# Kernel optimization log

Measured on AMD Instinct MI355X. Metric: run time of the kernel, lower is better.

The kernel has to match this reference:

```python
import jax, jax.numpy as jnp
import numpy as np

LEAK = 0.1
EPS = 1e-5


def setup_inputs() -> dict:
    key = jax.random.key(0)
    k1, k2, k3 = jax.random.split(key, 3)
    b, num1, num2, d_in, d_out, n_edges = 8, 4096, 4096, 256, 256, 262144
    N = num1 + num2
    x = jax.random.normal(k1, (b, N, d_in), dtype=jnp.float32)
    W = jax.random.normal(k2, (d_in, d_out), dtype=jnp.float32)
    edges = jax.random.randint(k3, (n_edges, 2), 0, N, dtype=jnp.int64)
    gamma = jnp.ones((d_out,), dtype=jnp.float32)   # LayerNorm weight
    beta = jnp.zeros((d_out,), dtype=jnp.float32)   # LayerNorm bias
    return {"x": x, "W": W, "gamma": gamma, "beta": beta,
            "edges": edges, "num1": num1, "num2": num2}


def reference(x, W, gamma, beta, edges, num1, num2):
    N = num1 + num2
    d_in, d_out = W.shape
    # edges2matrix: scatter 1.0 at (src, dst); duplicates just overwrite (set)
    adj = jnp.zeros((N, N), dtype=x.dtype).at[edges[:, 0], edges[:, 1]].set(1.0)
    # x <- A @ (x @ W), adjacency broadcast over batch
    h = jnp.einsum('nm,bmd->bnd', adj, x @ W)
    if d_out <= d_in:  # LeakyReLU(0.1) branch (static config)
        h = jnp.where(h >= 0, h, LEAK * h)
    # LayerNorm over last dim
    mean = jnp.mean(h, axis=-1, keepdims=True)
    var = jnp.var(h, axis=-1, keepdims=True)
    return gamma * (h - mean) * jax.lax.rsqrt(var + EPS) + beta
```

## Files before the change

### kernel.cpp

```cpp
#include <hip/hip_runtime.h>

#define N_NODES 8192
#define D 256
#define B 8
#define MAXDEG 128

typedef __attribute__((ext_vector_type(8))) short bf16x8;
typedef __attribute__((ext_vector_type(4))) float f32x4;
typedef __attribute__((ext_vector_type(4))) unsigned int u32x4;

static __device__ __forceinline__ float bf2f(unsigned short u) {
    union { float f; unsigned int i; } v; v.i = ((unsigned int)u) << 16; return v.f;
}
static __device__ __forceinline__ float bflo(unsigned int u) {
    union { float f; unsigned int i; } v; v.i = u << 16; return v.f;
}
static __device__ __forceinline__ float bfhi(unsigned int u) {
    union { float f; unsigned int i; } v; v.i = u & 0xFFFF0000u; return v.f;
}
static __device__ __forceinline__ unsigned short f2bf(float f) {
    union { float f; unsigned int i; } v; v.f = f;
    unsigned int r = v.i + 0x7FFFu + ((v.i >> 16) & 1u);
    return (unsigned short)(r >> 16);
}

__global__ __launch_bounds__(256) void build_csr(const int* __restrict__ edges,
        unsigned int* __restrict__ bitmask, int* __restrict__ deg,
        int* __restrict__ adj, int n_edges) {
    int i = blockIdx.x * 256 + threadIdx.x;
    if (i >= n_edges) return;
    int src = edges[2 * i];
    int dst = edges[2 * i + 1];
    unsigned int bitpos = (unsigned int)src * N_NODES + (unsigned int)dst;
    unsigned int bit = 1u << (bitpos & 31u);
    unsigned int old = atomicOr(&bitmask[bitpos >> 5], bit);
    if (!(old & bit)) {
        int slot = atomicAdd(&deg[src], 1);
        if (slot < MAXDEG) adj[src * MAXDEG + slot] = dst;
    }
}

__global__ __launch_bounds__(256) void convert_wt(const float* __restrict__ W,
        unsigned short* __restrict__ Wt) {
    int idx = blockIdx.x * 256 + threadIdx.x;
    int n = idx >> 8, k = idx & 255;
    Wt[n * 256 + k] = f2bf(W[k * 256 + n]);
}

#define GBM 128
__global__ __launch_bounds__(512) void gemm_mfma(const float* __restrict__ x,
        const unsigned short* __restrict__ Wt, unsigned short* __restrict__ xWb) {
    __shared__ alignas(16) char AsB[128 * 128];
    __shared__ alignas(16) char WsB[256 * 128];
    const int t = threadIdx.x;
    const int l = t & 63;
    const int w = t >> 6;
    const int wr = w >> 2;
    const int wc = w & 3;
    const size_t m0 = (size_t)blockIdx.x * GBM;

    f32x4 acc[4][4];
#pragma unroll
    for (int i = 0; i < 4; ++i)
#pragma unroll
        for (int j = 0; j < 4; ++j) acc[i][j] = (f32x4){0.f, 0.f, 0.f, 0.f};

    for (int ks = 0; ks < 4; ++ks) {
        const int k0 = ks * 64;
#pragma unroll
        for (int p = 0; p < 4; ++p) {
            const int row = p * 32 + (t >> 4);
            const int c4  = t & 15;
            float4 v = *(const float4*)&x[(m0 + row) * 256 + k0 + c4 * 4];
            uint2 pk;
            pk.x = (unsigned)f2bf(v.x) | ((unsigned)f2bf(v.y) << 16);
            pk.y = (unsigned)f2bf(v.z) | ((unsigned)f2bf(v.w) << 16);
            const int g = c4 >> 1;
            *(uint2*)&AsB[row * 128 + ((g ^ (row & 7)) * 16) + (c4 & 1) * 8] = pk;
        }
#pragma unroll
        for (int p = 0; p < 4; ++p) {
            const int rp = p * 64 + w * 8 + (l >> 3);
            const int sg = (l & 7) ^ (rp & 7);
            const unsigned short* gp = Wt + rp * 256 + k0 + sg * 8;
            char* lp = &WsB[p * 8192 + w * 1024];
            __builtin_amdgcn_global_load_lds(
                (__attribute__((address_space(1))) unsigned int*)gp,
                (__attribute__((address_space(3))) unsigned int*)lp, 16, 0, 0);
        }
        __syncthreads();
#pragma unroll
        for (int kc = 0; kc < 2; ++kc) {
            bf16x8 xa[4], wb[4];
#pragma unroll
            for (int fm = 0; fm < 4; ++fm) {
                const int row = wr * 64 + fm * 16 + (l & 15);
                const int g = kc * 4 + (l >> 4);
                xa[fm] = *(const bf16x8*)&AsB[row * 128 + ((g ^ (row & 7)) * 16)];
            }
#pragma unroll
            for (int fn = 0; fn < 4; ++fn) {
                const int n = wc * 64 + fn * 16 + (l & 15);
                const int g = kc * 4 + (l >> 4);
                wb[fn] = *(const bf16x8*)&WsB[n * 128 + ((g ^ (n & 7)) * 16)];
            }
#pragma unroll
            for (int fm = 0; fm < 4; ++fm)
#pragma unroll
                for (int fn = 0; fn < 4; ++fn)
                    acc[fm][fn] = __builtin_amdgcn_mfma_f32_16x16x32_bf16(
                        wb[fn], xa[fm], acc[fm][fn], 0, 0, 0);
        }
        __syncthreads();
    }
#pragma unroll
    for (int fm = 0; fm < 4; ++fm) {
        const size_t m = m0 + wr * 64 + fm * 16 + (l & 15);
        unsigned short* rowp = xWb + m * 256 + wc * 64 + (l >> 4) * 4;
#pragma unroll
        for (int fn = 0; fn < 4; ++fn) {
            f32x4 v = acc[fm][fn];
            uint2 pk;
            pk.x = (unsigned)f2bf(v.x) | ((unsigned)f2bf(v.y) << 16);
            pk.y = (unsigned)f2bf(v.z) | ((unsigned)f2bf(v.w) << 16);
            *(uint2*)(rowp + fn * 16) = pk;
        }
    }
}

__global__ __launch_bounds__(512) void gather_ln(const unsigned short* __restrict__ xWb,
        const int* __restrict__ deg, const int* __restrict__ adj,
        const float* __restrict__ gamma, const float* __restrict__ beta,
        float* __restrict__ out) {
    const int bid = blockIdx.x;
    const int batch = bid & 7;
    const int w = threadIdx.x >> 6;
    const int l = threadIdx.x & 63;
    const int half = l >> 5;
    const int sl = l & 31;
    const int n = (bid >> 3) * 8 + w;

    __shared__ int off[8][MAXDEG];
    int dg = deg[n];
    dg = dg > MAXDEG ? MAXDEG : dg;
    for (int i = l; i < dg; i += 64)
        off[w][i] = adj[n * MAXDEG + i] << 9;
    __syncthreads();

    const char* base = (const char*)xWb + (size_t)batch * (N_NODES * D * 2) + sl * 16;
    f32x4 a0 = {0.f, 0.f, 0.f, 0.f}, a1 = {0.f, 0.f, 0.f, 0.f};
    int i = 0;
#pragma unroll 2
    for (; i + 2 <= dg; i += 2) {
        u32x4 v = *(const u32x4*)(base + off[w][i + half]);
        f32x4 c0, c1;
        c0.x = bflo(v.x); c0.y = bfhi(v.x); c0.z = bflo(v.y); c0.w = bfhi(v.y);
        c1.x = bflo(v.z); c1.y = bfhi(v.z); c1.z = bflo(v.w); c1.w = bfhi(v.w);
        a0 += c0;
        a1 += c1;
    }
    if (i < dg && half == 0) {
        u32x4 v = *(const u32x4*)(base + off[w][i]);
        f32x4 c0, c1;
        c0.x = bflo(v.x); c0.y = bfhi(v.x); c0.z = bflo(v.y); c0.w = bfhi(v.y);
        c1.x = bflo(v.z); c1.y = bfhi(v.z); c1.z = bflo(v.w); c1.w = bfhi(v.w);
        a0 += c0;
        a1 += c1;
    }
    a0.x += __shfl_xor(a0.x, 32); a0.y += __shfl_xor(a0.y, 32);
    a0.z += __shfl_xor(a0.z, 32); a0.w += __shfl_xor(a0.w, 32);
    a1.x += __shfl_xor(a1.x, 32); a1.y += __shfl_xor(a1.y, 32);
    a1.z += __shfl_xor(a1.z, 32); a1.w += __shfl_xor(a1.w, 32);
    a0.x = a0.x >= 0.f ? a0.x : 0.1f * a0.x;
    a0.y = a0.y >= 0.f ? a0.y : 0.1f * a0.y;
    a0.z = a0.z >= 0.f ? a0.z : 0.1f * a0.z;
    a0.w = a0.w >= 0.f ? a0.w : 0.1f * a0.w;
    a1.x = a1.x >= 0.f ? a1.x : 0.1f * a1.x;
    a1.y = a1.y >= 0.f ? a1.y : 0.1f * a1.y;
    a1.z = a1.z >= 0.f ? a1.z : 0.1f * a1.z;
    a1.w = a1.w >= 0.f ? a1.w : 0.1f * a1.w;
    float s = (a0.x + a0.y + a0.z + a0.w) + (a1.x + a1.y + a1.z + a1.w);
    float q = (a0.x * a0.x + a0.y * a0.y + a0.z * a0.z + a0.w * a0.w)
            + (a1.x * a1.x + a1.y * a1.y + a1.z * a1.z + a1.w * a1.w);
#pragma unroll
    for (int o = 1; o < 32; o <<= 1) {
        s += __shfl_xor(s, o);
        q += __shfl_xor(q, o);
    }
    const float mean = s * (1.f / D);
    const float var  = q * (1.f / D) - mean * mean;
    const float rstd = rsqrtf(var + 1e-5f);
    f32x4 sel = half ? a1 : a0;
    const int col = sl * 8 + half * 4;
    float4 g  = *(const float4*)(gamma + col);
    float4 bt = *(const float4*)(beta + col);
    f32x4 o4;
    o4.x = g.x * (sel.x - mean) * rstd + bt.x;
    o4.y = g.y * (sel.y - mean) * rstd + bt.y;
    o4.z = g.z * (sel.z - mean) * rstd + bt.z;
    o4.w = g.w * (sel.w - mean) * rstd + bt.w;
    __builtin_nontemporal_store(o4,
        (f32x4*)(out + ((size_t)batch * N_NODES + n) * D + col));
}

extern "C" void kernel_launch(void* const* d_in, const int* in_sizes, int n_in,
                              void* d_out, int out_size, void* d_ws, size_t ws_size,
                              hipStream_t stream) {
    const float* x     = (const float*)d_in[0];
    const float* W     = (const float*)d_in[1];
    const float* gamma = (const float*)d_in[2];
    const float* beta  = (const float*)d_in[3];
    const int*   edges = (const int*)d_in[4];
    const int n_edges  = in_sizes[4] / 2;

    char* ws = (char*)d_ws;
    int*            degp    = (int*)ws;
    unsigned int*   bitmask = (unsigned int*)(ws + 32768);
    int*            adj     = (int*)(ws + 32768 + 8388608);
    unsigned short* xWb     = (unsigned short*)(ws + 32768 + 8388608 + 4194304);
    unsigned short* Wt      = (unsigned short*)(ws + 32768);

    (void)hipMemsetAsync(d_ws, 0, 32768 + 8388608, stream);

    build_csr<<<(n_edges + 255) / 256, 256, 0, stream>>>(edges, bitmask, degp, adj, n_edges);
    convert_wt<<<256, 256, 0, stream>>>(W, Wt);
    gemm_mfma<<<(B * N_NODES) / GBM, 512, 0, stream>>>(x, Wt, xWb);
    gather_ln<<<N_NODES, 512, 0, stream>>>(xWb, degp, adj, gamma, beta, (float*)d_out);
}
```

Measured before the change: 221.4 us.

## Pre-convert x to bf16 and load GEMM A tiles via direct global-to-LDS

Adds a separate convert_x kernel that writes x as bf16 into the output buffer, used as scratch. The GEMM can then stream A tiles with global_load_lds instead of loading fp32 and converting in registers. The gather kernel now stores neighbor offsets split by parity, so each half-wave walks its own list in a single unrolled loop with no tail branch. The cost is an extra kernel launch and an extra full pass over x: an fp32 read and a bf16 write, then a bf16 re-read.

```diff
diff --git a/kernel.cpp b/kernel.cpp
--- a/kernel.cpp
+++ b/kernel.cpp
@@ -9,19 +9,16 @@
 typedef __attribute__((ext_vector_type(4))) float f32x4;
 typedef __attribute__((ext_vector_type(4))) unsigned int u32x4;
 
-static __device__ __forceinline__ float bf2f(unsigned short u) {
-    union { float f; unsigned int i; } v; v.i = ((unsigned int)u) << 16; return v.f;
-}
 static __device__ __forceinline__ float bflo(unsigned int u) {
     union { float f; unsigned int i; } v; v.i = u << 16; return v.f;
 }
 static __device__ __forceinline__ float bfhi(unsigned int u) {
     union { float f; unsigned int i; } v; v.i = u & 0xFFFF0000u; return v.f;
 }
-static __device__ __forceinline__ unsigned short f2bf(float f) {
+static __device__ __forceinline__ unsigned int f2bf(float f) {
     union { float f; unsigned int i; } v; v.f = f;
     unsigned int r = v.i + 0x7FFFu + ((v.i >> 16) & 1u);
-    return (unsigned short)(r >> 16);
+    return r >> 16;
 }
 
 __global__ __launch_bounds__(256) void build_csr(const int* __restrict__ edges,
@@ -44,11 +41,24 @@
         unsigned short* __restrict__ Wt) {
     int idx = blockIdx.x * 256 + threadIdx.x;
     int n = idx >> 8, k = idx & 255;
-    Wt[n * 256 + k] = f2bf(W[k * 256 + n]);
+    Wt[n * 256 + k] = (unsigned short)f2bf(W[k * 256 + n]);
+}
+
+__global__ __launch_bounds__(256) void convert_x(const float* __restrict__ x,
+        unsigned short* __restrict__ xb) {
+    size_t i = ((size_t)blockIdx.x * 256 + threadIdx.x) * 8;
+    float4 v0 = *(const float4*)(x + i);
+    float4 v1 = *(const float4*)(x + i + 4);
+    u32x4 o;
+    o.x = f2bf(v0.x) | (f2bf(v0.y) << 16);
+    o.y = f2bf(v0.z) | (f2bf(v0.w) << 16);
+    o.z = f2bf(v1.x) | (f2bf(v1.y) << 16);
+    o.w = f2bf(v1.z) | (f2bf(v1.w) << 16);
+    *(u32x4*)(xb + i) = o;
 }
 
 #define GBM 128
-__global__ __launch_bounds__(512) void gemm_mfma(const float* __restrict__ x,
+__global__ __launch_bounds__(512) void gemm_mfma(const unsigned short* __restrict__ xb,
         const unsigned short* __restrict__ Wt, unsigned short* __restrict__ xWb) {
     __shared__ alignas(16) char AsB[128 * 128];
     __shared__ alignas(16) char WsB[256 * 128];
@@ -68,15 +78,14 @@
     for (int ks = 0; ks < 4; ++ks) {
         const int k0 = ks * 64;
 #pragma unroll
-        for (int p = 0; p < 4; ++p) {
-            const int row = p * 32 + (t >> 4);
-            const int c4  = t & 15;
-            float4 v = *(const float4*)&x[(m0 + row) * 256 + k0 + c4 * 4];
-            uint2 pk;
-            pk.x = (unsigned)f2bf(v.x) | ((unsigned)f2bf(v.y) << 16);
-            pk.y = (unsigned)f2bf(v.z) | ((unsigned)f2bf(v.w) << 16);
-            const int g = c4 >> 1;
-            *(uint2*)&AsB[row * 128 + ((g ^ (row & 7)) * 16) + (c4 & 1) * 8] = pk;
+        for (int p = 0; p < 2; ++p) {
+            const int row = p * 64 + w * 8 + (l >> 3);
+            const int sg = (l & 7) ^ (row & 7);
+            const unsigned short* gp = xb + (m0 + row) * 256 + k0 + sg * 8;
+            char* lp = &AsB[p * 8192 + w * 1024];
+            __builtin_amdgcn_global_load_lds(
+                (__attribute__((address_space(1))) unsigned int*)gp,
+                (__attribute__((address_space(3))) unsigned int*)lp, 16, 0, 0);
         }
 #pragma unroll
         for (int p = 0; p < 4; ++p) {
@@ -121,8 +130,8 @@
         for (int fn = 0; fn < 4; ++fn) {
             f32x4 v = acc[fm][fn];
             uint2 pk;
-            pk.x = (unsigned)f2bf(v.x) | ((unsigned)f2bf(v.y) << 16);
-            pk.y = (unsigned)f2bf(v.z) | ((unsigned)f2bf(v.w) << 16);
+            pk.x = f2bf(v.x) | (f2bf(v.y) << 16);
+            pk.y = f2bf(v.z) | (f2bf(v.w) << 16);
             *(uint2*)(rowp + fn * 16) = pk;
         }
     }
@@ -140,27 +149,20 @@
     const int sl = l & 31;
     const int n = (bid >> 3) * 8 + w;
 
-    __shared__ int off[8][MAXDEG];
+    __shared__ int off[8][2][64];
     int dg = deg[n];
     dg = dg > MAXDEG ? MAXDEG : dg;
     for (int i = l; i < dg; i += 64)
-        off[w][i] = adj[n * MAXDEG + i] << 9;
+        off[w][i & 1][i >> 1] = adj[n * MAXDEG + i] << 9;
     __syncthreads();
 
-    const char* base = (const char*)xWb + (size_t)batch * (N_NODES * D * 2) + sl * 16;
+    const char* slab = (const char*)xWb + (size_t)batch * (N_NODES * D * 2);
+    const int sl16 = sl * 16;
+    const int jn = (dg - half + 1) >> 1;
     f32x4 a0 = {0.f, 0.f, 0.f, 0.f}, a1 = {0.f, 0.f, 0.f, 0.f};
-    int i = 0;
-#pragma unroll 2
-    for (; i + 2 <= dg; i += 2) {
-        u32x4 v = *(const u32x4*)(base + off[w][i + half]);
-        f32x4 c0, c1;
-        c0.x = bflo(v.x); c0.y = bfhi(v.x); c0.z = bflo(v.y); c0.w = bfhi(v.y);
-        c1.x = bflo(v.z); c1.y = bfhi(v.z); c1.z = bflo(v.w); c1.w = bfhi(v.w);
-        a0 += c0;
-        a1 += c1;
-    }
-    if (i < dg && half == 0) {
-        u32x4 v = *(const u32x4*)(base + off[w][i]);
+#pragma unroll 4
+    for (int j = 0; j < jn; ++j) {
+        u32x4 v = *(const u32x4*)(slab + (unsigned)(off[w][half][j] + sl16));
         f32x4 c0, c1;
         c0.x = bflo(v.x); c0.y = bfhi(v.x); c0.z = bflo(v.y); c0.w = bfhi(v.y);
         c1.x = bflo(v.z); c1.y = bfhi(v.z); c1.z = bflo(v.w); c1.w = bfhi(v.w);
@@ -219,11 +221,13 @@
     int*            adj     = (int*)(ws + 32768 + 8388608);
     unsigned short* xWb     = (unsigned short*)(ws + 32768 + 8388608 + 4194304);
     unsigned short* Wt      = (unsigned short*)(ws + 32768);
+    unsigned short* xb      = (unsigned short*)d_out;
 
     (void)hipMemsetAsync(d_ws, 0, 32768 + 8388608, stream);
 
     build_csr<<<(n_edges + 255) / 256, 256, 0, stream>>>(edges, bitmask, degp, adj, n_edges);
     convert_wt<<<256, 256, 0, stream>>>(W, Wt);
-    gemm_mfma<<<(B * N_NODES) / GBM, 512, 0, stream>>>(x, Wt, xWb);
+    convert_x<<<8192, 256, 0, stream>>>(x, xb);
+    gemm_mfma<<<(B * N_NODES) / GBM, 512, 0, stream>>>(xb, Wt, xWb);
     gather_ln<<<N_NODES, 512, 0, stream>>>(xWb, degp, adj, gamma, beta, (float*)d_out);
 }
```

Result: no change. 223.2 us (+0.8%).
